# Kernel optimization log

Hardware: AMD Instinct MI355X
Metric: run time of the kernel (lower is better)

Reference implementation:

```python
import jax, jax.numpy as jnp
import numpy as np

B, C, H, W = 32, 512, 32, 32
TXT_DIM, M, NUM_HEADS = 768, 77, 8
HEAD_DIM = C // NUM_HEADS
SCALE = HEAD_DIM ** -0.5


def setup_inputs() -> dict:
    key = jax.random.key(0)
    ks = jax.random.split(key, 9)
    x = jax.random.normal(ks[0], (B, C, H, W), dtype=jnp.float32)
    text_emb = jax.random.normal(ks[1], (B, M, TXT_DIM), dtype=jnp.float32)
    attention_mask = jnp.ones((B, M), dtype=jnp.int32)
    # Linear params (PyTorch convention: weight [out, in], bias [out])
    s_q = 1.0 / np.sqrt(C)
    s_kv = 1.0 / np.sqrt(TXT_DIM)
    Wq = jax.random.uniform(ks[2], (C, C), jnp.float32, -s_q, s_q)
    bq = jax.random.uniform(ks[3], (C,), jnp.float32, -s_q, s_q)
    Wk = jax.random.uniform(ks[4], (C, TXT_DIM), jnp.float32, -s_kv, s_kv)
    bk = jax.random.uniform(ks[5], (C,), jnp.float32, -s_kv, s_kv)
    Wv = jax.random.uniform(ks[6], (C, TXT_DIM), jnp.float32, -s_kv, s_kv)
    bv = jax.random.uniform(ks[7], (C,), jnp.float32, -s_kv, s_kv)
    return {"x": x, "text_emb": text_emb, "attention_mask": attention_mask,
            "Wq": Wq, "bq": bq, "Wk": Wk, "bk": bk, "Wv": Wv, "bv": bv}


def reference(x, text_emb, attention_mask, Wq, bq, Wk, bk, Wv, bv):
    b, c, h, w = x.shape
    n = h * w
    x_flat = x.reshape(b, c, n).transpose(0, 2, 1)          # [B, N, C]
    Q = x_flat @ Wq.T + bq                                   # [B, N, C]
    K = text_emb @ Wk.T + bk                                 # [B, M, C]
    V = text_emb @ Wv.T + bv                                 # [B, M, C]
    Q = Q.reshape(b, n, NUM_HEADS, HEAD_DIM)
    K = K.reshape(b, -1, NUM_HEADS, HEAD_DIM)
    V = V.reshape(b, -1, NUM_HEADS, HEAD_DIM)
    # scores: [B, heads, N, M]
    scores = jnp.einsum('bnhd,bmhd->bhnm', Q, K) * SCALE
    mask = attention_mask[:, None, None, :] != 0
    scores = jnp.where(mask, scores, -jnp.inf)
    probs = jax.nn.softmax(scores, axis=-1)
    out = jnp.einsum('bhnm,bmhd->bnhd', probs, V)            # [B, N, heads, d]
    out = out.reshape(b, n, c).transpose(0, 2, 1).reshape(b, c, h, w)
    return out
```

## Files before the change

kernel.cpp:

```cpp
#include <hip/hip_runtime.h>
#include <math.h>

#define BB   32
#define CC   512
#define HWN  1024
#define MM   77
#define TXT  768
#define NH   8
#define HD   64
#define SCALEF 0.125f
#define MPAD 96
#define KVROWS (BB*MPAD)
#define PP   104
#define OSP  132

typedef __attribute__((ext_vector_type(8))) short          bf16x8;
typedef __attribute__((ext_vector_type(8))) unsigned short us8;
typedef __attribute__((ext_vector_type(4))) float          f32x4;

__device__ inline unsigned short f2bf(float f) {
    union { float f; unsigned u; } v; v.f = f;
    unsigned r = v.u + 0x7fff + ((v.u >> 16) & 1);
    return (unsigned short)(r >> 16);
}

__device__ inline void gload_lds16(const void* g, void* l) {
    __builtin_amdgcn_global_load_lds(
        (const __attribute__((address_space(1))) void*)g,
        (__attribute__((address_space(3))) void*)l, 16, 0, 0);
}

#define TGRID 4096
#define CV_WQ 65536
#define CV_WK 98304
#define CV_WV 98304
#define CV_TE 473088
#define CVTOT (CV_WQ + CV_WK + CV_WV + CV_TE)

__global__ __launch_bounds__(256) void prep_kernel(
    const float* __restrict__ x, const float* __restrict__ te,
    const float* __restrict__ Wq, const float* __restrict__ Wk,
    const float* __restrict__ Wv,
    unsigned short* __restrict__ xT, unsigned short* __restrict__ teb,
    unsigned short* __restrict__ Wqb, unsigned short* __restrict__ Wkb,
    unsigned short* __restrict__ Wvb)
{
    const int bid = blockIdx.x;
    const int t = threadIdx.x;

    if (bid < TGRID) {
        const int nt = bid & 15, ct = (bid >> 4) & 7, b = bid >> 7;
        const int n0 = nt * 64, c0 = ct * 64;
        __shared__ float tile[64][65];
        const float* xb = x + (size_t)b * CC * HWN;
        {
            const int c = t >> 2;
            #pragma unroll
            for (int j = 0; j < 4; ++j) {
                const int f4 = (t & 3) + j * 4;
                const float4 v = *(const float4*)&xb[(size_t)(c0 + c) * HWN + n0 + f4 * 4];
                tile[c][f4 * 4 + 0] = v.x; tile[c][f4 * 4 + 1] = v.y;
                tile[c][f4 * 4 + 2] = v.z; tile[c][f4 * 4 + 3] = v.w;
            }
        }
        __syncthreads();
        unsigned short* xTb = xT + (size_t)b * HWN * CC;
        #pragma unroll
        for (int j = 0; j < 2; ++j) {
            const int n = (t >> 3) + j * 32;
            const int c8 = (t & 7) * 8;
            us8 o;
            #pragma unroll
            for (int i = 0; i < 8; ++i) o[i] = f2bf(tile[c8 + i][n]);
            *(us8*)&xTb[(size_t)(n0 + n) * CC + c0 + c8] = o;
        }
    } else {
        const int idx = (bid - TGRID) * 256 + t;
        const float* src; unsigned short* dst; int off;
        if (idx < CV_WQ)                    { src = Wq; dst = Wqb; off = idx; }
        else if (idx < CV_WQ + CV_WK)       { src = Wk; dst = Wkb; off = idx - CV_WQ; }
        else if (idx < CV_WQ + CV_WK + CV_WV) { src = Wv; dst = Wvb; off = idx - CV_WQ - CV_WK; }
        else                                { src = te; dst = teb; off = idx - CV_WQ - CV_WK - CV_WV; }
        const float4 v = ((const float4*)src)[off];
        ushort4 o;
        o.x = f2bf(v.x); o.y = f2bf(v.y); o.z = f2bf(v.z); o.w = f2bf(v.w);
        ((ushort4*)dst)[off] = o;
    }
}

__global__ __launch_bounds__(256) void gemm_all(
    const unsigned short* __restrict__ xT, const unsigned short* __restrict__ Wqb,
    const float* __restrict__ bq, unsigned short* __restrict__ Qb,
    const unsigned short* __restrict__ teb,
    const unsigned short* __restrict__ Wkb, const float* __restrict__ bk,
    const unsigned short* __restrict__ Wvb, const float* __restrict__ bv,
    unsigned short* __restrict__ Kb, unsigned short* __restrict__ Vt)
{
    const int bid = blockIdx.x;
    __shared__ unsigned short As[128 * 32];
    __shared__ unsigned short Bs[128 * 32];
    const int t = threadIdx.x;
    const int lane = t & 63, w = t >> 6;
    const int wr = w >> 1, wc = w & 1;
    const int lm = lane & 15, quad = lane >> 4;
    const int lrow = lane >> 2, lk = (lane & 3) * 8;

    const unsigned short *gA0, *gA1, *gB0, *gB1;
    int kIters, mode, row0, co0;

    if (bid < 1024) {
        mode = 0;
        const int rt = bid & 255, ct = bid >> 8;
        row0 = rt * 128; co0 = ct * 128;
        kIters = CC / 32;
        gA0 = xT  + (size_t)(row0 + (w * 2 + 0) * 16 + lrow) * CC + lk;
        gA1 = xT  + (size_t)(row0 + (w * 2 + 1) * 16 + lrow) * CC + lk;
        gB0 = Wqb + (size_t)(co0 + (w * 2 + 0) * 16 + lrow) * CC + lk;
        gB1 = Wqb + (size_t)(co0 + (w * 2 + 1) * 16 + lrow) * CC + lk;
    } else {
        const int id = bid - 1024;
        const int rt = id % 24, cc = id / 24;
        const int isV = (cc >= 4);
        mode = isV ? 2 : 1;
        row0 = rt * 128; co0 = (cc & 3) * 128;
        kIters = TXT / 32;
        const unsigned short* Wb = isV ? Wvb : Wkb;
        const int rp0 = row0 + (w * 2 + 0) * 16 + lrow;
        const int rp1 = row0 + (w * 2 + 1) * 16 + lrow;
        const int b0i = rp0 / MPAD, m0i = min(rp0 % MPAD, MM - 1);
        const int b1i = rp1 / MPAD, m1i = min(rp1 % MPAD, MM - 1);
        gA0 = teb + (size_t)(b0i * MM + m0i) * TXT + lk;
        gA1 = teb + (size_t)(b1i * MM + m1i) * TXT + lk;
        gB0 = Wb + (size_t)(co0 + (w * 2 + 0) * 16 + lrow) * TXT + lk;
        gB1 = Wb + (size_t)(co0 + (w * 2 + 1) * 16 + lrow) * TXT + lk;
    }

    f32x4 acc[4][4] = {};

    for (int k = 0; k < kIters; ++k) {
        gload_lds16(gA0 + k * 32, &As[(w * 2 + 0) * 512]);
        gload_lds16(gA1 + k * 32, &As[(w * 2 + 1) * 512]);
        gload_lds16(gB0 + k * 32, &Bs[(w * 2 + 0) * 512]);
        gload_lds16(gB1 + k * 32, &Bs[(w * 2 + 1) * 512]);
        __syncthreads();
        bf16x8 a[4], bfr[4];
        #pragma unroll
        for (int i = 0; i < 4; ++i)
            a[i] = *(const bf16x8*)&As[(wr * 64 + i * 16 + lm) * 32 + quad * 8];
        #pragma unroll
        for (int i = 0; i < 4; ++i)
            bfr[i] = *(const bf16x8*)&Bs[(wc * 64 + i * 16 + lm) * 32 + quad * 8];
        #pragma unroll
        for (int mi = 0; mi < 4; ++mi)
            #pragma unroll
            for (int ni = 0; ni < 4; ++ni)
                acc[mi][ni] = __builtin_amdgcn_mfma_f32_16x16x32_bf16(
                    a[mi], bfr[ni], acc[mi][ni], 0, 0, 0);
        __syncthreads();
    }

    if (mode == 0) {
        #pragma unroll
        for (int ni = 0; ni < 4; ++ni) {
            const int col = co0 + wc * 64 + ni * 16 + lm;
            const float bias = bq[col];
            #pragma unroll
            for (int mi = 0; mi < 4; ++mi) {
                #pragma unroll
                for (int j = 0; j < 4; ++j) {
                    const int row = row0 + wr * 64 + mi * 16 + quad * 4 + j;
                    Qb[(size_t)row * CC + col] = f2bf(acc[mi][ni][j] + bias);
                }
            }
        }
    } else {
        const float* bias_p = (mode == 2) ? bv : bk;
        #pragma unroll
        for (int ni = 0; ni < 4; ++ni) {
            const int col = co0 + wc * 64 + ni * 16 + lm;
            const float bias = bias_p[col];
            #pragma unroll
            for (int mi = 0; mi < 4; ++mi) {
                #pragma unroll
                for (int j = 0; j < 4; ++j) {
                    const int row = row0 + wr * 64 + mi * 16 + quad * 4 + j;
                    const int bo = row / MPAD, mo = row % MPAD;
                    const unsigned short hv = f2bf(acc[mi][ni][j] + bias);
                    if (mode == 2) {
                        Vt[((size_t)bo * CC + col) * MPAD + mo] = hv;
                    } else if (mo < MM) {
                        Kb[((size_t)bo * MM + mo) * CC + col] = hv;
                    }
                }
            }
        }
    }
}

__global__ __launch_bounds__(256) void attn_mfma(
    const unsigned short* __restrict__ Qb, const unsigned short* __restrict__ Kb,
    const unsigned short* __restrict__ Vt, const int* __restrict__ amask,
    float* __restrict__ out)
{
    const int ntile = blockIdx.x;
    const int h     = blockIdx.y;
    const int b     = blockIdx.z;
    const int row0  = ntile * 128;

    __shared__ char smem[64 * OSP * 4];
    __shared__ float msk[80];
    unsigned short* Ps = (unsigned short*)smem;
    float* Os = (float*)smem;

    const int t = threadIdx.x;
    const int w = t >> 6, lane = t & 63;
    const int lm = lane & 15, quad = lane >> 4;

    {
        const int r = t >> 1, off = 80 + (t & 1) * 8;
        us8 z = {0, 0, 0, 0, 0, 0, 0, 0};
        *(us8*)&Ps[r * PP + off] = z;
    }
    if (t < 80) msk[t] = (t < MM && amask[b * MM + t] != 0) ? 0.f : -INFINITY;
    __syncthreads();

    f32x4 s[2][5] = {};
    const unsigned short* qbase = Qb + ((size_t)b * HWN + row0) * CC + h * HD;
    const unsigned short* kbase = Kb + (size_t)b * MM * CC + h * HD;
    #pragma unroll
    for (int ks = 0; ks < 2; ++ks) {
        bf16x8 a[2], kf[5];
        #pragma unroll
        for (int mt = 0; mt < 2; ++mt)
            a[mt] = *(const bf16x8*)&qbase[(size_t)((w * 2 + mt) * 16 + lm) * CC + ks * 32 + quad * 8];
        #pragma unroll
        for (int n = 0; n < 5; ++n) {
            const int kr = min(n * 16 + lm, MM - 1);
            kf[n] = *(const bf16x8*)&kbase[(size_t)kr * CC + ks * 32 + quad * 8];
        }
        #pragma unroll
        for (int mt = 0; mt < 2; ++mt)
            #pragma unroll
            for (int n = 0; n < 5; ++n)
                s[mt][n] = __builtin_amdgcn_mfma_f32_16x16x32_bf16(a[mt], kf[n], s[mt][n], 0, 0, 0);
    }

    float inv[2][4];
    #pragma unroll
    for (int mt = 0; mt < 2; ++mt) {
        #pragma unroll
        for (int j = 0; j < 4; ++j) {
            float v[5];
            #pragma unroll
            for (int n = 0; n < 5; ++n)
                v[n] = s[mt][n][j] * SCALEF + msk[n * 16 + lm];
            float mx = fmaxf(fmaxf(fmaxf(v[0], v[1]), fmaxf(v[2], v[3])), v[4]);
            mx = fmaxf(mx, __shfl_xor(mx, 1, 64));
            mx = fmaxf(mx, __shfl_xor(mx, 2, 64));
            mx = fmaxf(mx, __shfl_xor(mx, 4, 64));
            mx = fmaxf(mx, __shfl_xor(mx, 8, 64));
            float sum = 0.f;
            #pragma unroll
            for (int n = 0; n < 5; ++n) { v[n] = __expf(v[n] - mx); sum += v[n]; }
            sum += __shfl_xor(sum, 1, 64);
            sum += __shfl_xor(sum, 2, 64);
            sum += __shfl_xor(sum, 4, 64);
            sum += __shfl_xor(sum, 8, 64);
            inv[mt][j] = 1.0f / sum;
            const int mrow = (w * 2 + mt) * 16 + quad * 4 + j;
            #pragma unroll
            for (int n = 0; n < 5; ++n)
                Ps[mrow * PP + n * 16 + lm] = f2bf(v[n]);
        }
    }
    __syncthreads();

    f32x4 o[2][4] = {};
    const unsigned short* vbase = Vt + ((size_t)b * CC + h * HD) * MPAD;
    #pragma unroll
    for (int ks = 0; ks < 3; ++ks) {
        bf16x8 a[2], vf[4];
        #pragma unroll
        for (int mt = 0; mt < 2; ++mt)
            a[mt] = *(const bf16x8*)&Ps[((w * 2 + mt) * 16 + lm) * PP + ks * 32 + quad * 8];
        #pragma unroll
        for (int n = 0; n < 4; ++n)
            vf[n] = *(const bf16x8*)&vbase[(size_t)(n * 16 + lm) * MPAD + ks * 32 + quad * 8];
        #pragma unroll
        for (int mt = 0; mt < 2; ++mt)
            #pragma unroll
            for (int n = 0; n < 4; ++n)
                o[mt][n] = __builtin_amdgcn_mfma_f32_16x16x32_bf16(a[mt], vf[n], o[mt][n], 0, 0, 0);
    }
    __syncthreads();

    #pragma unroll
    for (int mt = 0; mt < 2; ++mt) {
        #pragma unroll
        for (int n = 0; n < 4; ++n) {
            const int col = n * 16 + lm;
            const int r0 = (w * 2 + mt) * 16 + quad * 4;
            float4 st;
            st.x = o[mt][n][0] * inv[mt][0];
            st.y = o[mt][n][1] * inv[mt][1];
            st.z = o[mt][n][2] * inv[mt][2];
            st.w = o[mt][n][3] * inv[mt][3];
            *(float4*)&Os[col * OSP + r0] = st;
        }
    }
    __syncthreads();

    float* obase = out + ((size_t)b * CC + h * HD) * HWN + row0;
    #pragma unroll
    for (int p = 0; p < 8; ++p) {
        const int idx = p * 256 + t;
        const int col = idx >> 5;
        const int r4  = idx & 31;
        const float4 v = *(const float4*)&Os[col * OSP + r4 * 4];
        *(float4*)&obase[(size_t)col * HWN + r4 * 4] = v;
    }
}

extern "C" void kernel_launch(void* const* d_in, const int* in_sizes, int n_in,
                              void* d_out, int out_size, void* d_ws, size_t ws_size,
                              hipStream_t stream)
{
    const float* x     = (const float*)d_in[0];
    const float* te    = (const float*)d_in[1];
    const int*   amask = (const int*)d_in[2];
    const float* Wq    = (const float*)d_in[3];
    const float* bq    = (const float*)d_in[4];
    const float* Wk    = (const float*)d_in[5];
    const float* bk    = (const float*)d_in[6];
    const float* Wv    = (const float*)d_in[7];
    const float* bv    = (const float*)d_in[8];
    float* out = (float*)d_out;

    unsigned short* xT  = (unsigned short*)d_ws;
    unsigned short* Qb  = xT  + (size_t)BB * HWN * CC;
    unsigned short* Kb  = Qb  + (size_t)BB * HWN * CC;
    unsigned short* Vt  = Kb  + (size_t)BB * MM * CC;
    unsigned short* Wqb = Vt  + (size_t)BB * CC * MPAD;
    unsigned short* Wkb = Wqb + (size_t)CC * CC;
    unsigned short* Wvb = Wkb + (size_t)CC * TXT;
    unsigned short* teb = Wvb + (size_t)CC * TXT;

    prep_kernel<<<dim3(TGRID + CVTOT / 256), 256, 0, stream>>>(
        x, te, Wq, Wk, Wv, xT, teb, Wqb, Wkb, Wvb);
    gemm_all<<<dim3(1024 + 192), 256, 0, stream>>>(
        xT, Wqb, bq, Qb, teb, Wkb, bk, Wvb, bv, Kb, Vt);
    attn_mfma<<<dim3(8, NH, BB), 256, 0, stream>>>(Qb, Kb, Vt, amask, out);
}
```

Baseline: 224.9 us.

## Triple-buffer LDS tiles in projection GEMM with two-stage prefetch

The projection GEMM kernel now keeps three LDS buffers for A and B tiles and issues global-to-LDS loads two K-steps ahead. Manual vmcnt waits and a single barrier per iteration replace the two __syncthreads per step. The aim is to hide global memory latency behind MFMA work. In exchange it triples the kernel's LDS use, which can cut occupancy, and it depends on hand-written waitcnt ordering being correct.

```diff
diff --git a/kernel.cpp b/kernel.cpp
--- a/kernel.cpp
+++ b/kernel.cpp
@@ -97,8 +97,8 @@
     unsigned short* __restrict__ Kb, unsigned short* __restrict__ Vt)
 {
     const int bid = blockIdx.x;
-    __shared__ unsigned short As[128 * 32];
-    __shared__ unsigned short Bs[128 * 32];
+    __shared__ unsigned short As[3][128 * 32];
+    __shared__ unsigned short Bs[3][128 * 32];
     const int t = threadIdx.x;
     const int lane = t & 63, w = t >> 6;
     const int wr = w >> 1, wc = w & 1;
@@ -137,26 +137,50 @@
 
     f32x4 acc[4][4] = {};
 
+    const int lA0 = (w * 2 + 0) * 512, lA1 = (w * 2 + 1) * 512;
+
+    gload_lds16(gA0, &As[0][lA0]);
+    gload_lds16(gA1, &As[0][lA1]);
+    gload_lds16(gB0, &Bs[0][lA0]);
+    gload_lds16(gB1, &Bs[0][lA1]);
+    gload_lds16(gA0 + 32, &As[1][lA0]);
+    gload_lds16(gA1 + 32, &As[1][lA1]);
+    gload_lds16(gB0 + 32, &Bs[1][lA0]);
+    gload_lds16(gB1 + 32, &Bs[1][lA1]);
+
+    int cb = 0;
     for (int k = 0; k < kIters; ++k) {
-        gload_lds16(gA0 + k * 32, &As[(w * 2 + 0) * 512]);
-        gload_lds16(gA1 + k * 32, &As[(w * 2 + 1) * 512]);
-        gload_lds16(gB0 + k * 32, &Bs[(w * 2 + 0) * 512]);
-        gload_lds16(gB1 + k * 32, &Bs[(w * 2 + 1) * 512]);
-        __syncthreads();
+        if (k == kIters - 1) {
+            asm volatile("s_waitcnt vmcnt(0)" ::: "memory");
+        } else {
+            asm volatile("s_waitcnt vmcnt(4)" ::: "memory");
+        }
+        __builtin_amdgcn_s_barrier();
+        __builtin_amdgcn_sched_barrier(0);
+
+        if (k + 2 < kIters) {
+            const int nb = (cb >= 1) ? cb - 1 : 2;
+            gload_lds16(gA0 + (k + 2) * 32, &As[nb][lA0]);
+            gload_lds16(gA1 + (k + 2) * 32, &As[nb][lA1]);
+            gload_lds16(gB0 + (k + 2) * 32, &Bs[nb][lA0]);
+            gload_lds16(gB1 + (k + 2) * 32, &Bs[nb][lA1]);
+        }
+
         bf16x8 a[4], bfr[4];
         #pragma unroll
         for (int i = 0; i < 4; ++i)
-            a[i] = *(const bf16x8*)&As[(wr * 64 + i * 16 + lm) * 32 + quad * 8];
+            a[i] = *(const bf16x8*)&As[cb][(wr * 64 + i * 16 + lm) * 32 + quad * 8];
         #pragma unroll
         for (int i = 0; i < 4; ++i)
-            bfr[i] = *(const bf16x8*)&Bs[(wc * 64 + i * 16 + lm) * 32 + quad * 8];
+            bfr[i] = *(const bf16x8*)&Bs[cb][(wc * 64 + i * 16 + lm) * 32 + quad * 8];
         #pragma unroll
         for (int mi = 0; mi < 4; ++mi)
             #pragma unroll
             for (int ni = 0; ni < 4; ++ni)
                 acc[mi][ni] = __builtin_amdgcn_mfma_f32_16x16x32_bf16(
                     a[mi], bfr[ni], acc[mi][ni], 0, 0, 0);
-        __syncthreads();
+
+        cb = (cb >= 2) ? 0 : cb + 1;
     }
 
     if (mode == 0) {
```

Result: faster. 219.0 us (-2.6%).
